# Performance work log

Hardware: AMD Instinct MI355X
Metric: run time of the kernel (lower is better)

The kernel has to match this reference:

```python
import jax, jax.numpy as jnp
import numpy as np

B, S, D = 4, 2048, 1024
CTX_LEN, CTX_DIM = 77, 768
H, DH = 16, 64
INNER = H * DH
MULT = 4
EPS = 1e-5


def setup_inputs() -> dict:
    key = jax.random.key(0)
    ks = jax.random.split(key, 14)
    nrm = lambda k, shape: jax.random.normal(k, shape, dtype=jnp.float32) * 0.02
    return {
        "x": jax.random.normal(ks[0], (B, S, D), dtype=jnp.float32),
        "context": jax.random.normal(ks[1], (B, CTX_LEN, CTX_DIM), dtype=jnp.float32),
        "ln1_g": jnp.ones((D,), jnp.float32), "ln1_b": jnp.zeros((D,), jnp.float32),
        "ln2_g": jnp.ones((D,), jnp.float32), "ln2_b": jnp.zeros((D,), jnp.float32),
        "ln3_g": jnp.ones((D,), jnp.float32), "ln3_b": jnp.zeros((D,), jnp.float32),
        "a1_wq": nrm(ks[2], (D, INNER)), "a1_wk": nrm(ks[3], (D, INNER)),
        "a1_wv": nrm(ks[4], (D, INNER)), "a1_wo": nrm(ks[5], (INNER, D)),
        "a1_bo": jnp.zeros((D,), jnp.float32),
        "a2_wq": nrm(ks[6], (D, INNER)), "a2_wk": nrm(ks[7], (CTX_DIM, INNER)),
        "a2_wv": nrm(ks[8], (CTX_DIM, INNER)), "a2_wo": nrm(ks[9], (INNER, D)),
        "a2_bo": jnp.zeros((D,), jnp.float32),
        "ff_w1": nrm(ks[10], (D, D * MULT * 2)), "ff_b1": jnp.zeros((D * MULT * 2,), jnp.float32),
        "ff_w2": nrm(ks[11], (D * MULT, D)), "ff_b2": jnp.zeros((D,), jnp.float32),
    }


def _layernorm(x, g, b):
    mu = jnp.mean(x, axis=-1, keepdims=True)
    var = jnp.var(x, axis=-1, keepdims=True)
    return (x - mu) * jax.lax.rsqrt(var + EPS) * g + b


def _attn(xq, xkv, wq, wk, wv, wo, bo):
    b, sq, _ = xq.shape
    sk = xkv.shape[1]
    q = (xq @ wq).reshape(b, sq, H, DH)
    k = (xkv @ wk).reshape(b, sk, H, DH)
    v = (xkv @ wv).reshape(b, sk, H, DH)
    score = jnp.einsum('bqhd,bkhd->bhqk', q, k) * (DH ** -0.5)
    w = jax.nn.softmax(score, axis=-1)
    o = jnp.einsum('bhqk,bkhd->bqhd', w, v).reshape(b, sq, INNER)
    return o @ wo + bo


def _block(x, context, ln1_g, ln1_b, ln2_g, ln2_b, ln3_g, ln3_b,
           a1_wq, a1_wk, a1_wv, a1_wo, a1_bo,
           a2_wq, a2_wk, a2_wv, a2_wo, a2_bo,
           ff_w1, ff_b1, ff_w2, ff_b2):
    # self-attention
    x = _attn(_layernorm(x, ln1_g, ln1_b), _layernorm(x, ln1_g, ln1_b),
              a1_wq, a1_wk, a1_wv, a1_wo, a1_bo) + x
    # cross-attention
    x = _attn(_layernorm(x, ln2_g, ln2_b), context,
              a2_wq, a2_wk, a2_wv, a2_wo, a2_bo) + x
    # GeGLU feed-forward
    h = _layernorm(x, ln3_g, ln3_b) @ ff_w1 + ff_b1
    u, gate = jnp.split(h, 2, axis=-1)
    x = (u * jax.nn.gelu(gate, approximate=False)) @ ff_w2 + ff_b2 + x
    return x


def reference(x, context, ln1_g, ln1_b, ln2_g, ln2_b, ln3_g, ln3_b,
              a1_wq, a1_wk, a1_wv, a1_wo, a1_bo,
              a2_wq, a2_wk, a2_wv, a2_wo, a2_bo,
              ff_w1, ff_b1, ff_w2, ff_b2):
    return _block(x, context, ln1_g, ln1_b, ln2_g, ln2_b, ln3_g, ln3_b,
                  a1_wq, a1_wk, a1_wv, a1_wo, a1_bo,
                  a2_wq, a2_wk, a2_wv, a2_wo, a2_bo,
                  ff_w1, ff_b1, ff_w2, ff_b2)
```

## Files before the change

kernel.cpp:

```cpp
#include <hip/hip_runtime.h>
#include <hip/hip_bf16.h>
#include <math.h>

typedef __bf16 bf16;
typedef __bf16 bf16x8 __attribute__((ext_vector_type(8)));
typedef float f32x4 __attribute__((ext_vector_type(4)));

#define MFMA(a, b, c) __builtin_amdgcn_mfma_f32_16x16x32_bf16((a), (b), (c), 0, 0, 0)

static __device__ __forceinline__ void gl16(const bf16* g, bf16* l) {
  __builtin_amdgcn_global_load_lds(
      (const __attribute__((address_space(1))) void*)g,
      (__attribute__((address_space(3))) void*)l, 16, 0, 0);
}

static __device__ __forceinline__ bf16x8 bzero8() {
  bf16x8 v;
#pragma unroll
  for (int i = 0; i < 8; ++i) v[i] = (bf16)0.0f;
  return v;
}

__global__ void k_transpose_cvt(const float* __restrict__ W, bf16* __restrict__ Wt,
                                int K, int N) {
  __shared__ float tile[32][33];
  int k0 = blockIdx.x * 32, n0 = blockIdx.y * 32;
  int tx = threadIdx.x & 31, ty = threadIdx.x >> 5;
  for (int i = ty; i < 32; i += 8)
    tile[i][tx] = W[(size_t)(k0 + i) * N + (n0 + tx)];
  __syncthreads();
  for (int i = ty; i < 32; i += 8)
    Wt[(size_t)(n0 + i) * K + (k0 + tx)] = (bf16)tile[tx][i];
}

__global__ void k_transpose_v(const bf16* __restrict__ V, bf16* __restrict__ Vt,
                              int rows, int kvpad) {
  __shared__ __attribute__((aligned(16))) bf16 tile[64][72];
  int t0 = blockIdx.x * 64, h = blockIdx.y, b = blockIdx.z;
  int t = threadIdx.x;
  int tr = t >> 2, c0 = (t & 3) * 16;
  int token = t0 + tr;
  bf16x8 a = bzero8(), bv = bzero8();
  if (token < rows) {
    const bf16* src = V + ((size_t)(b * rows + token)) * 1024 + h * 64 + c0;
    a = *(const bf16x8*)src;
    bv = *(const bf16x8*)(src + 8);
  }
  *(bf16x8*)&tile[tr][c0] = a;
  *(bf16x8*)&tile[tr][c0 + 8] = bv;
  __syncthreads();
  int d = t >> 2, tq = (t & 3) * 16;
  bf16x8 o1, o2;
#pragma unroll
  for (int i = 0; i < 8; ++i) { o1[i] = tile[tq + i][d]; o2[i] = tile[tq + 8 + i][d]; }
  bf16* dst = Vt + ((size_t)((b * 16 + h) * 64 + d)) * kvpad + t0 + tq;
  *(bf16x8*)dst = o1;
  *(bf16x8*)(dst + 8) = o2;
}

__global__ void k_cvt(const float* __restrict__ in, bf16* __restrict__ out, int n) {
  int i = blockIdx.x * 256 + threadIdx.x;
  if (i < n) out[i] = (bf16)in[i];
}

__global__ void k_layernorm(const float* __restrict__ x, const float* __restrict__ g,
                            const float* __restrict__ b, bf16* __restrict__ out) {
  int row = blockIdx.x;
  float4 v = ((const float4*)(x + (size_t)row * 1024))[threadIdx.x];
  float s = v.x + v.y + v.z + v.w;
  float ss = v.x * v.x + v.y * v.y + v.z * v.z + v.w * v.w;
#pragma unroll
  for (int off = 1; off < 64; off <<= 1) {
    s += __shfl_xor(s, off);
    ss += __shfl_xor(ss, off);
  }
  __shared__ float sm[4], sm2[4];
  int w = threadIdx.x >> 6;
  if ((threadIdx.x & 63) == 0) { sm[w] = s; sm2[w] = ss; }
  __syncthreads();
  s = sm[0] + sm[1] + sm[2] + sm[3];
  ss = sm2[0] + sm2[1] + sm2[2] + sm2[3];
  float mu = s * (1.0f / 1024.0f);
  float var = ss * (1.0f / 1024.0f) - mu * mu;
  float rs = rsqrtf(var + 1e-5f);
  float4 gg = ((const float4*)g)[threadIdx.x];
  float4 bb = ((const float4*)b)[threadIdx.x];
  bf16* o = out + (size_t)row * 1024 + threadIdx.x * 4;
  o[0] = (bf16)((v.x - mu) * rs * gg.x + bb.x);
  o[1] = (bf16)((v.y - mu) * rs * gg.y + bb.y);
  o[2] = (bf16)((v.z - mu) * rs * gg.z + bb.z);
  o[3] = (bf16)((v.w - mu) * rs * gg.w + bb.w);
}

template <int EPI>
__global__ __launch_bounds__(256, 2)
void k_gemm_bt(const bf16* __restrict__ A, const bf16* __restrict__ Bt,
               const float* __restrict__ bias, const float* __restrict__ res,
               void* __restrict__ Cp, int M, int N, int K) {
  __shared__ __attribute__((aligned(16))) bf16 As[128 * 32];
  __shared__ __attribute__((aligned(16))) bf16 Bs[128 * 32];
  int m0 = blockIdx.x * 128, n0 = blockIdx.y * 128;
  int tid = threadIdx.x, lane = tid & 63, wave = tid >> 6;
  int wm = (wave >> 1) * 64, wn = (wave & 1) * 64;
  int quad = lane >> 4, l15 = lane & 15;
  f32x4 acc[4][4];
#pragma unroll
  for (int i = 0; i < 4; ++i)
#pragma unroll
    for (int j = 0; j < 4; ++j)
#pragma unroll
      for (int r = 0; r < 4; ++r) acc[i][j][r] = 0.0f;
  int srow = wave * 16 + (lane >> 2), scol = (lane & 3) * 8;
  const bf16* ga = A + (size_t)(m0 + srow) * K + scol;
  const bf16* gb = Bt + (size_t)(n0 + srow) * K + scol;
  bf16* la = As + srow * 32 + scol;
  bf16* lb = Bs + srow * 32 + scol;
  for (int k0 = 0; k0 < K; k0 += 32) {
    gl16(ga, la);
    gl16(ga + (size_t)64 * K, la + 64 * 32);
    gl16(gb, lb);
    gl16(gb + (size_t)64 * K, lb + 64 * 32);
    ga += 32; gb += 32;
    __syncthreads();
    bf16x8 af[4], bfr[4];
#pragma unroll
    for (int i = 0; i < 4; ++i) af[i] = *(const bf16x8*)(&As[(wm + i * 16 + l15) * 32 + quad * 8]);
#pragma unroll
    for (int i = 0; i < 4; ++i) bfr[i] = *(const bf16x8*)(&Bs[(wn + i * 16 + l15) * 32 + quad * 8]);
#pragma unroll
    for (int mi = 0; mi < 4; ++mi)
#pragma unroll
      for (int ni = 0; ni < 4; ++ni)
        acc[mi][ni] = MFMA(af[mi], bfr[ni], acc[mi][ni]);
    __syncthreads();
  }
#pragma unroll
  for (int mi = 0; mi < 4; ++mi) {
#pragma unroll
    for (int r = 0; r < 4; ++r) {
      int row = m0 + wm + mi * 16 + quad * 4 + r;
      if (row >= M) continue;
#pragma unroll
      for (int ni = 0; ni < 4; ++ni) {
        int col = n0 + wn + ni * 16 + l15;
        float v = acc[mi][ni][r];
        if (EPI == 0) {
          ((bf16*)Cp)[(size_t)row * N + col] = (bf16)v;
        } else {
          ((float*)Cp)[(size_t)row * N + col] =
              v + bias[col] + res[(size_t)row * N + col];
        }
      }
    }
  }
}

__global__ __launch_bounds__(256, 2)
void k_gemm_geglu(const bf16* __restrict__ A, const bf16* __restrict__ W1t,
                  const float* __restrict__ b1, bf16* __restrict__ Hg,
                  int M, int K) {
  __shared__ __attribute__((aligned(16))) bf16 As[128 * 32];
  __shared__ __attribute__((aligned(16))) bf16 Bu[128 * 32];
  __shared__ __attribute__((aligned(16))) bf16 Bg[128 * 32];
  const int N = 4096;
  int m0 = blockIdx.x * 128, n0 = blockIdx.y * 128;
  int tid = threadIdx.x, lane = tid & 63, wave = tid >> 6;
  int wm = (wave >> 1) * 64, wn = (wave & 1) * 64;
  int quad = lane >> 4, l15 = lane & 15;
  f32x4 accu[4][4], accg[4][4];
#pragma unroll
  for (int i = 0; i < 4; ++i)
#pragma unroll
    for (int j = 0; j < 4; ++j)
#pragma unroll
      for (int r = 0; r < 4; ++r) { accu[i][j][r] = 0.0f; accg[i][j][r] = 0.0f; }
  int srow = wave * 16 + (lane >> 2), scol = (lane & 3) * 8;
  const bf16* ga = A + (size_t)(m0 + srow) * K + scol;
  const bf16* gu = W1t + (size_t)(n0 + srow) * K + scol;
  const bf16* gg = W1t + (size_t)(n0 + srow + 4096) * K + scol;
  bf16* la = As + srow * 32 + scol;
  bf16* lu = Bu + srow * 32 + scol;
  bf16* lg = Bg + srow * 32 + scol;
  for (int k0 = 0; k0 < K; k0 += 32) {
    gl16(ga, la);
    gl16(ga + (size_t)64 * K, la + 64 * 32);
    gl16(gu, lu);
    gl16(gu + (size_t)64 * K, lu + 64 * 32);
    gl16(gg, lg);
    gl16(gg + (size_t)64 * K, lg + 64 * 32);
    ga += 32; gu += 32; gg += 32;
    __syncthreads();
    bf16x8 af[4], bu[4], bg[4];
#pragma unroll
    for (int i = 0; i < 4; ++i) af[i] = *(const bf16x8*)(&As[(wm + i * 16 + l15) * 32 + quad * 8]);
#pragma unroll
    for (int i = 0; i < 4; ++i) bu[i] = *(const bf16x8*)(&Bu[(wn + i * 16 + l15) * 32 + quad * 8]);
#pragma unroll
    for (int i = 0; i < 4; ++i) bg[i] = *(const bf16x8*)(&Bg[(wn + i * 16 + l15) * 32 + quad * 8]);
#pragma unroll
    for (int mi = 0; mi < 4; ++mi)
#pragma unroll
      for (int ni = 0; ni < 4; ++ni) {
        accu[mi][ni] = MFMA(af[mi], bu[ni], accu[mi][ni]);
        accg[mi][ni] = MFMA(af[mi], bg[ni], accg[mi][ni]);
      }
    __syncthreads();
  }
#pragma unroll
  for (int mi = 0; mi < 4; ++mi)
#pragma unroll
    for (int r = 0; r < 4; ++r) {
      int row = m0 + wm + mi * 16 + quad * 4 + r;
#pragma unroll
      for (int ni = 0; ni < 4; ++ni) {
        int col = n0 + wn + ni * 16 + l15;
        float u = accu[mi][ni][r] + b1[col];
        float g = accg[mi][ni][r] + b1[col + 4096];
        float ge = 0.5f * g * (1.0f + erff(g * 0.70710678118654752f));
        Hg[(size_t)row * N + col] = (bf16)(u * ge);
      }
    }
}

__global__ __launch_bounds__(256, 2)
void k_flash(const bf16* __restrict__ Q, const bf16* __restrict__ Kb,
             const bf16* __restrict__ VtG, bf16* __restrict__ O,
             int Sq, int Sk, int kvrows, int kvpad) {
  __shared__ __attribute__((aligned(16))) bf16 Ks[64][72];
  __shared__ __attribute__((aligned(16))) bf16 Vs[64][72];
  __shared__ __attribute__((aligned(16))) bf16 Ps[4][16][72];
  int qt = blockIdx.x, h = blockIdx.y, b = blockIdx.z;
  int tid = threadIdx.x, lane = tid & 63, wave = tid >> 6;
  int quad = lane >> 4, l15 = lane & 15;
  const bf16* qsrc = Q + (size_t)(b * Sq + qt * 64 + wave * 16 + l15) * 1024 + h * 64 + quad * 8;
  bf16x8 aq0 = *(const bf16x8*)qsrc;
  bf16x8 aq1 = *(const bf16x8*)(qsrc + 32);
  bf16x8 ones8;
#pragma unroll
  for (int i = 0; i < 8; ++i) ones8[i] = (bf16)1.0f;

  float m_r[4], l_r[4];
  f32x4 acc_o[4];
#pragma unroll
  for (int r = 0; r < 4; ++r) { m_r[r] = -1e30f; l_r[r] = 0.0f; }
#pragma unroll
  for (int ni = 0; ni < 4; ++ni)
#pragma unroll
    for (int r = 0; r < 4; ++r) acc_o[ni][r] = 0.0f;

  int tr = tid >> 2, c0 = (tid & 3) * 16;
  const bf16* vrow = VtG + ((size_t)((b * 16 + h) * 64 + tr)) * kvpad + c0;

  for (int k0 = 0; k0 < Sk; k0 += 64) {
    {
      int krow = k0 + tr;
      bf16x8 k1 = bzero8(), k2 = bzero8();
      if (krow < Sk) {
        const bf16* ks = Kb + (size_t)(b * kvrows + krow) * 1024 + h * 64 + c0;
        k1 = *(const bf16x8*)ks;
        k2 = *(const bf16x8*)(ks + 8);
      }
      *(bf16x8*)(&Ks[tr][c0]) = k1;
      *(bf16x8*)(&Ks[tr][c0 + 8]) = k2;
      bf16x8 v1 = *(const bf16x8*)(vrow + k0);
      bf16x8 v2 = *(const bf16x8*)(vrow + k0 + 8);
      *(bf16x8*)(&Vs[tr][c0]) = v1;
      *(bf16x8*)(&Vs[tr][c0 + 8]) = v2;
    }
    __syncthreads();

    f32x4 sacc[4];
#pragma unroll
    for (int ni = 0; ni < 4; ++ni)
#pragma unroll
      for (int r = 0; r < 4; ++r) sacc[ni][r] = 0.0f;
#pragma unroll
    for (int ni = 0; ni < 4; ++ni) {
      bf16x8 bk0 = *(const bf16x8*)(&Ks[ni * 16 + l15][quad * 8]);
      bf16x8 bk1 = *(const bf16x8*)(&Ks[ni * 16 + l15][32 + quad * 8]);
      sacc[ni] = MFMA(aq0, bk0, sacc[ni]);
      sacc[ni] = MFMA(aq1, bk1, sacc[ni]);
    }
    float s_v[4][4];
#pragma unroll
    for (int ni = 0; ni < 4; ++ni)
#pragma unroll
      for (int r = 0; r < 4; ++r) {
        float sv = sacc[ni][r] * 0.125f;
        if (k0 + ni * 16 + l15 >= Sk) sv = -1e30f;
        s_v[ni][r] = sv;
      }
    float alpha[4];
#pragma unroll
    for (int r = 0; r < 4; ++r) {
      float v = fmaxf(fmaxf(s_v[0][r], s_v[1][r]), fmaxf(s_v[2][r], s_v[3][r]));
#pragma unroll
      for (int off = 1; off < 16; off <<= 1) v = fmaxf(v, __shfl_xor(v, off));
      float mn = fmaxf(m_r[r], v);
      alpha[r] = __expf(m_r[r] - mn);
      m_r[r] = mn;
    }
#pragma unroll
    for (int ni = 0; ni < 4; ++ni)
#pragma unroll
      for (int r = 0; r < 4; ++r)
        Ps[wave][quad * 4 + r][ni * 16 + l15] = (bf16)__expf(s_v[ni][r] - m_r[r]);
    bf16x8 ap0 = *(const bf16x8*)(&Ps[wave][l15][quad * 8]);
    bf16x8 ap1 = *(const bf16x8*)(&Ps[wave][l15][32 + quad * 8]);
    f32x4 psum;
#pragma unroll
    for (int r = 0; r < 4; ++r) psum[r] = 0.0f;
    psum = MFMA(ap0, ones8, psum);
    psum = MFMA(ap1, ones8, psum);
#pragma unroll
    for (int r = 0; r < 4; ++r) l_r[r] = l_r[r] * alpha[r] + psum[r];
#pragma unroll
    for (int ni = 0; ni < 4; ++ni) {
#pragma unroll
      for (int r = 0; r < 4; ++r) acc_o[ni][r] *= alpha[r];
      bf16x8 bv0 = *(const bf16x8*)(&Vs[ni * 16 + l15][quad * 8]);
      bf16x8 bv1 = *(const bf16x8*)(&Vs[ni * 16 + l15][32 + quad * 8]);
      acc_o[ni] = MFMA(ap0, bv0, acc_o[ni]);
      acc_o[ni] = MFMA(ap1, bv1, acc_o[ni]);
    }
    __syncthreads();
  }
#pragma unroll
  for (int ni = 0; ni < 4; ++ni)
#pragma unroll
    for (int r = 0; r < 4; ++r) {
      int q = qt * 64 + wave * 16 + quad * 4 + r;
      float ov = acc_o[ni][r] / l_r[r];
      O[(size_t)(b * Sq + q) * 1024 + h * 64 + ni * 16 + l15] = (bf16)ov;
    }
}

extern "C" void kernel_launch(void* const* d_in, const int* in_sizes, int n_in,
                              void* d_out, int out_size, void* d_ws, size_t ws_size,
                              hipStream_t stream) {
  (void)in_sizes; (void)n_in; (void)out_size; (void)ws_size;
  const float* x = (const float*)d_in[0];
  const float* ctx = (const float*)d_in[1];
  const float* ln1_g = (const float*)d_in[2];
  const float* ln1_b = (const float*)d_in[3];
  const float* ln2_g = (const float*)d_in[4];
  const float* ln2_b = (const float*)d_in[5];
  const float* ln3_g = (const float*)d_in[6];
  const float* ln3_b = (const float*)d_in[7];
  const float* a1_wq = (const float*)d_in[8];
  const float* a1_wk = (const float*)d_in[9];
  const float* a1_wv = (const float*)d_in[10];
  const float* a1_wo = (const float*)d_in[11];
  const float* a1_bo = (const float*)d_in[12];
  const float* a2_wq = (const float*)d_in[13];
  const float* a2_wk = (const float*)d_in[14];
  const float* a2_wv = (const float*)d_in[15];
  const float* a2_wo = (const float*)d_in[16];
  const float* a2_bo = (const float*)d_in[17];
  const float* ff_w1 = (const float*)d_in[18];
  const float* ff_b1 = (const float*)d_in[19];
  const float* ff_w2 = (const float*)d_in[20];
  const float* ff_b2 = (const float*)d_in[21];
  float* xout = (float*)d_out;

  const int M = 4 * 2048;
  char* ws = (char*)d_ws;
  size_t off = 0;
  auto alloc = [&](size_t elems) -> bf16* {
    bf16* p = (bf16*)(ws + off);
    off += ((elems * sizeof(bf16)) + 255) & ~(size_t)255;
    return p;
  };
  bf16* wq1t = alloc((size_t)1024 * 1024);
  bf16* wk1t = alloc((size_t)1024 * 1024);
  bf16* wv1t = alloc((size_t)1024 * 1024);
  bf16* wo1t = alloc((size_t)1024 * 1024);
  bf16* wq2t = alloc((size_t)1024 * 1024);
  bf16* wk2t = alloc((size_t)1024 * 768);
  bf16* wv2t = alloc((size_t)1024 * 768);
  bf16* wo2t = alloc((size_t)1024 * 1024);
  bf16* w1t = alloc((size_t)8192 * 1024);
  bf16* w2t = alloc((size_t)1024 * 4096);
  bf16* lnb = alloc((size_t)M * 1024);
  bf16* qb = alloc((size_t)M * 1024);
  bf16* kb = alloc((size_t)M * 1024);
  bf16* vb = alloc((size_t)M * 1024);
  bf16* ab = alloc((size_t)M * 1024);
  bf16* ctxb = alloc((size_t)308 * 768);
  bf16* kcb = alloc((size_t)308 * 1024);
  bf16* vcb = alloc((size_t)308 * 1024);
  bf16* hgb = alloc((size_t)M * 4096);
  bf16* vtb = hgb;
  bf16* vtcb = hgb + (size_t)4 * 16 * 64 * 2048;

  hipMemcpyAsync(xout, x, (size_t)M * 1024 * sizeof(float),
                 hipMemcpyDeviceToDevice, stream);

  k_transpose_cvt<<<dim3(32, 32), 256, 0, stream>>>(a1_wq, wq1t, 1024, 1024);
  k_transpose_cvt<<<dim3(32, 32), 256, 0, stream>>>(a1_wk, wk1t, 1024, 1024);
  k_transpose_cvt<<<dim3(32, 32), 256, 0, stream>>>(a1_wv, wv1t, 1024, 1024);
  k_transpose_cvt<<<dim3(32, 32), 256, 0, stream>>>(a1_wo, wo1t, 1024, 1024);
  k_transpose_cvt<<<dim3(32, 32), 256, 0, stream>>>(a2_wq, wq2t, 1024, 1024);
  k_transpose_cvt<<<dim3(24, 32), 256, 0, stream>>>(a2_wk, wk2t, 768, 1024);
  k_transpose_cvt<<<dim3(24, 32), 256, 0, stream>>>(a2_wv, wv2t, 768, 1024);
  k_transpose_cvt<<<dim3(32, 32), 256, 0, stream>>>(a2_wo, wo2t, 1024, 1024);
  k_transpose_cvt<<<dim3(32, 256), 256, 0, stream>>>(ff_w1, w1t, 1024, 8192);
  k_transpose_cvt<<<dim3(128, 32), 256, 0, stream>>>(ff_w2, w2t, 4096, 1024);
  k_cvt<<<(308 * 768 + 255) / 256, 256, 0, stream>>>(ctx, ctxb, 308 * 768);

  k_layernorm<<<M, 256, 0, stream>>>(xout, ln1_g, ln1_b, lnb);
  k_gemm_bt<0><<<dim3(64, 8), 256, 0, stream>>>(lnb, wq1t, nullptr, nullptr, qb, M, 1024, 1024);
  k_gemm_bt<0><<<dim3(64, 8), 256, 0, stream>>>(lnb, wk1t, nullptr, nullptr, kb, M, 1024, 1024);
  k_gemm_bt<0><<<dim3(64, 8), 256, 0, stream>>>(lnb, wv1t, nullptr, nullptr, vb, M, 1024, 1024);
  k_transpose_v<<<dim3(32, 16, 4), 256, 0, stream>>>(vb, vtb, 2048, 2048);
  k_flash<<<dim3(32, 16, 4), 256, 0, stream>>>(qb, kb, vtb, ab, 2048, 2048, 2048, 2048);
  k_gemm_bt<1><<<dim3(64, 8), 256, 0, stream>>>(ab, wo1t, a1_bo, xout, xout, M, 1024, 1024);

  k_layernorm<<<M, 256, 0, stream>>>(xout, ln2_g, ln2_b, lnb);
  k_gemm_bt<0><<<dim3(64, 8), 256, 0, stream>>>(lnb, wq2t, nullptr, nullptr, qb, M, 1024, 1024);
  k_gemm_bt<0><<<dim3(3, 8), 256, 0, stream>>>(ctxb, wk2t, nullptr, nullptr, kcb, 308, 1024, 768);
  k_gemm_bt<0><<<dim3(3, 8), 256, 0, stream>>>(ctxb, wv2t, nullptr, nullptr, vcb, 308, 1024, 768);
  k_transpose_v<<<dim3(2, 16, 4), 256, 0, stream>>>(vcb, vtcb, 77, 128);
  k_flash<<<dim3(32, 16, 4), 256, 0, stream>>>(qb, kcb, vtcb, ab, 2048, 77, 77, 128);
  k_gemm_bt<1><<<dim3(64, 8), 256, 0, stream>>>(ab, wo2t, a2_bo, xout, xout, M, 1024, 1024);

  k_layernorm<<<M, 256, 0, stream>>>(xout, ln3_g, ln3_b, lnb);
  k_gemm_geglu<<<dim3(64, 32), 256, 0, stream>>>(lnb, w1t, ff_b1, hgb, M, 1024);
  k_gemm_bt<1><<<dim3(64, 8), 256, 0, stream>>>(hgb, w2t, ff_b2, xout, xout, M, 1024, 4096);
}
```

Measured before the change: 930.7 us.

## Double-buffer flash attention K/V tiles with async LDS loads and XOR swizzle

Rewrites the flash-attention K/V staging to use global_load_lds directly into double-buffered, XOR-swizzled shared tiles. The next tile is prefetched while the current one is computed, which removes one barrier per iteration and hides load latency. It also switches to exp2 with a pre-folded scale constant, applies the bounds mask only on the tail tile, and raises the occupancy hint to 4 blocks per CU. Risks: the K rows past Sk are no longer zero-filled, so reads beyond kvrows depend on padding. The larger LDS footprint and the register cap from the higher launch bound could cause spills.

```diff
diff --git a/kernel.cpp b/kernel.cpp
--- a/kernel.cpp
+++ b/kernel.cpp
@@ -222,13 +222,14 @@
     }
 }
 
-__global__ __launch_bounds__(256, 2)
+#define CSC 0.18033688011112042f
+__global__ __launch_bounds__(256, 4)
 void k_flash(const bf16* __restrict__ Q, const bf16* __restrict__ Kb,
              const bf16* __restrict__ VtG, bf16* __restrict__ O,
              int Sq, int Sk, int kvrows, int kvpad) {
-  __shared__ __attribute__((aligned(16))) bf16 Ks[64][72];
-  __shared__ __attribute__((aligned(16))) bf16 Vs[64][72];
-  __shared__ __attribute__((aligned(16))) bf16 Ps[4][16][72];
+  __shared__ __attribute__((aligned(16))) bf16 Ks[2][64 * 64];
+  __shared__ __attribute__((aligned(16))) bf16 Vs[2][64 * 64];
+  __shared__ __attribute__((aligned(16))) bf16 Ps[4][16 * 64];
   int qt = blockIdx.x, h = blockIdx.y, b = blockIdx.z;
   int tid = threadIdx.x, lane = tid & 63, wave = tid >> 6;
   int quad = lane >> 4, l15 = lane & 15;
@@ -248,26 +249,33 @@
 #pragma unroll
     for (int r = 0; r < 4; ++r) acc_o[ni][r] = 0.0f;
 
-  int tr = tid >> 2, c0 = (tid & 3) * 16;
-  const bf16* vrow = VtG + ((size_t)((b * 16 + h) * 64 + tr)) * kvpad + c0;
-
-  for (int k0 = 0; k0 < Sk; k0 += 64) {
-    {
-      int krow = k0 + tr;
-      bf16x8 k1 = bzero8(), k2 = bzero8();
-      if (krow < Sk) {
-        const bf16* ks = Kb + (size_t)(b * kvrows + krow) * 1024 + h * 64 + c0;
-        k1 = *(const bf16x8*)ks;
-        k2 = *(const bf16x8*)(ks + 8);
-      }
-      *(bf16x8*)(&Ks[tr][c0]) = k1;
-      *(bf16x8*)(&Ks[tr][c0 + 8]) = k2;
-      bf16x8 v1 = *(const bf16x8*)(vrow + k0);
-      bf16x8 v2 = *(const bf16x8*)(vrow + k0 + 8);
-      *(bf16x8*)(&Vs[tr][c0]) = v1;
-      *(bf16x8*)(&Vs[tr][c0 + 8]) = v2;
-    }
-    __syncthreads();
+  int srow = tid >> 3;
+  int scol = ((tid & 7) * 8) ^ ((srow & 7) << 3);
+  const bf16* kg0 = Kb + (size_t)(b * kvrows + srow) * 1024 + h * 64 + scol;
+  const bf16* vg0 = VtG + ((size_t)((b * 16 + h) * 64 + srow)) * kvpad + scol;
+
+  int nt = (Sk + 63) >> 6;
+  {
+    gl16(kg0, &Ks[0][tid * 8]);
+    gl16(kg0 + (size_t)32 * 1024, &Ks[0][2048 + tid * 8]);
+    gl16(vg0, &Vs[0][tid * 8]);
+    gl16(vg0 + (size_t)32 * kvpad, &Vs[0][2048 + tid * 8]);
+  }
+  __syncthreads();
+
+  int cur = 0;
+  for (int t = 0; t < nt; ++t) {
+    int k0 = t << 6;
+    if (t + 1 < nt) {
+      const bf16* kg = kg0 + (size_t)(k0 + 64) * 1024;
+      const bf16* vg = vg0 + (k0 + 64);
+      gl16(kg, &Ks[cur ^ 1][tid * 8]);
+      gl16(kg + (size_t)32 * 1024, &Ks[cur ^ 1][2048 + tid * 8]);
+      gl16(vg, &Vs[cur ^ 1][tid * 8]);
+      gl16(vg + (size_t)32 * kvpad, &Vs[cur ^ 1][2048 + tid * 8]);
+    }
+    const bf16* Kc = &Ks[cur][0];
+    const bf16* Vc = &Vs[cur][0];
 
     f32x4 sacc[4];
 #pragma unroll
@@ -276,37 +284,47 @@
       for (int r = 0; r < 4; ++r) sacc[ni][r] = 0.0f;
 #pragma unroll
     for (int ni = 0; ni < 4; ++ni) {
-      bf16x8 bk0 = *(const bf16x8*)(&Ks[ni * 16 + l15][quad * 8]);
-      bf16x8 bk1 = *(const bf16x8*)(&Ks[ni * 16 + l15][32 + quad * 8]);
+      int krow = ni * 16 + l15;
+      int sw = (krow & 7) << 3;
+      bf16x8 bk0 = *(const bf16x8*)&Kc[krow * 64 + ((quad * 8) ^ sw)];
+      bf16x8 bk1 = *(const bf16x8*)&Kc[krow * 64 + ((32 + quad * 8) ^ sw)];
       sacc[ni] = MFMA(aq0, bk0, sacc[ni]);
       sacc[ni] = MFMA(aq1, bk1, sacc[ni]);
     }
-    float s_v[4][4];
-#pragma unroll
-    for (int ni = 0; ni < 4; ++ni)
-#pragma unroll
-      for (int r = 0; r < 4; ++r) {
-        float sv = sacc[ni][r] * 0.125f;
-        if (k0 + ni * 16 + l15 >= Sk) sv = -1e30f;
-        s_v[ni][r] = sv;
+    if (k0 + 64 > Sk) {
+#pragma unroll
+      for (int ni = 0; ni < 4; ++ni) {
+        bool oob = (k0 + ni * 16 + l15 >= Sk);
+#pragma unroll
+        for (int r = 0; r < 4; ++r)
+          if (oob) sacc[ni][r] = -1e30f;
       }
-    float alpha[4];
+    }
+    float alpha[4], mC[4];
 #pragma unroll
     for (int r = 0; r < 4; ++r) {
-      float v = fmaxf(fmaxf(s_v[0][r], s_v[1][r]), fmaxf(s_v[2][r], s_v[3][r]));
+      float v = fmaxf(fmaxf(sacc[0][r], sacc[1][r]), fmaxf(sacc[2][r], sacc[3][r]));
 #pragma unroll
       for (int off = 1; off < 16; off <<= 1) v = fmaxf(v, __shfl_xor(v, off));
       float mn = fmaxf(m_r[r], v);
-      alpha[r] = __expf(m_r[r] - mn);
+      alpha[r] = __builtin_amdgcn_exp2f((m_r[r] - mn) * CSC);
       m_r[r] = mn;
-    }
-#pragma unroll
-    for (int ni = 0; ni < 4; ++ni)
-#pragma unroll
-      for (int r = 0; r < 4; ++r)
-        Ps[wave][quad * 4 + r][ni * 16 + l15] = (bf16)__expf(s_v[ni][r] - m_r[r]);
-    bf16x8 ap0 = *(const bf16x8*)(&Ps[wave][l15][quad * 8]);
-    bf16x8 ap1 = *(const bf16x8*)(&Ps[wave][l15][32 + quad * 8]);
+      mC[r] = mn * CSC;
+    }
+    bf16* ps = &Ps[wave][0];
+#pragma unroll
+    for (int ni = 0; ni < 4; ++ni) {
+      int col = ni * 16 + l15;
+#pragma unroll
+      for (int r = 0; r < 4; ++r) {
+        int prow = quad * 4 + r;
+        ps[prow * 64 + (col ^ ((prow & 7) << 3))] =
+            (bf16)__builtin_amdgcn_exp2f(sacc[ni][r] * CSC - mC[r]);
+      }
+    }
+    int swp = (l15 & 7) << 3;
+    bf16x8 ap0 = *(const bf16x8*)&ps[l15 * 64 + ((quad * 8) ^ swp)];
+    bf16x8 ap1 = *(const bf16x8*)&ps[l15 * 64 + ((32 + quad * 8) ^ swp)];
     f32x4 psum;
 #pragma unroll
     for (int r = 0; r < 4; ++r) psum[r] = 0.0f;
@@ -318,12 +336,15 @@
     for (int ni = 0; ni < 4; ++ni) {
 #pragma unroll
       for (int r = 0; r < 4; ++r) acc_o[ni][r] *= alpha[r];
-      bf16x8 bv0 = *(const bf16x8*)(&Vs[ni * 16 + l15][quad * 8]);
-      bf16x8 bv1 = *(const bf16x8*)(&Vs[ni * 16 + l15][32 + quad * 8]);
+      int vrow = ni * 16 + l15;
+      int sw = (vrow & 7) << 3;
+      bf16x8 bv0 = *(const bf16x8*)&Vc[vrow * 64 + ((quad * 8) ^ sw)];
+      bf16x8 bv1 = *(const bf16x8*)&Vc[vrow * 64 + ((32 + quad * 8) ^ sw)];
       acc_o[ni] = MFMA(ap0, bv0, acc_o[ni]);
       acc_o[ni] = MFMA(ap1, bv1, acc_o[ni]);
     }
     __syncthreads();
+    cur ^= 1;
   }
 #pragma unroll
   for (int ni = 0; ni < 4; ++ni)
```

New measurement: 901.4 us. 3.2% less time.
